# Performance work log

Hardware: AMD Instinct MI355X
Metric: run time of the kernel (lower is better)

The kernel has to match this reference:

```python
import jax, jax.numpy as jnp
import numpy as np

B, N, NODE_DIM = 256, 200, 2
H, D, L, FF = 8, 128, 3, 512
KD = D // H  # key/val dim per head = 16
EPS = 1e-5


def _uniform(key, shape, fan):
    s = 1.0 / np.sqrt(fan)
    return jax.random.uniform(key, shape, jnp.float32, -s, s)


def setup_inputs() -> dict:
    key = jax.random.key(0)
    ks = jax.random.split(key, 16)
    return {
        "x": jax.random.normal(ks[0], (B, N, NODE_DIM), jnp.float32),
        "Wemb": _uniform(ks[1], (NODE_DIM, D), NODE_DIM),
        "bemb": _uniform(ks[2], (D,), NODE_DIM),
        "Wq": _uniform(ks[3], (L, H, D, KD), KD),
        "Wk": _uniform(ks[4], (L, H, D, KD), KD),
        "Wv": _uniform(ks[5], (L, H, D, KD), KD),
        "Wo": _uniform(ks[6], (L, H, KD, D), D),
        "bn1_g": jnp.ones((L, D), jnp.float32),
        "bn1_b": jnp.zeros((L, D), jnp.float32),
        "W1": _uniform(ks[7], (L, D, FF), D),
        "b1": _uniform(ks[8], (L, FF), D),
        "W2": _uniform(ks[9], (L, FF, D), FF),
        "b2": _uniform(ks[10], (L, D), FF),
        "bn2_g": jnp.ones((L, D), jnp.float32),
        "bn2_b": jnp.zeros((L, D), jnp.float32),
    }


def _batch_norm(h, g, b):
    # BatchNorm1d in training mode: stats over all (batch*graph) positions per channel
    hf = h.reshape(-1, h.shape[-1])
    m = hf.mean(axis=0)
    v = hf.var(axis=0)  # biased variance, as torch uses for normalization
    return (h - m) * jax.lax.rsqrt(v + EPS) * g + b


def _mha(h, Wq, Wk, Wv, Wo):
    # h: [B,N,D]; Wq/Wk/Wv: [H,D,KD]; Wo: [H,KD,D]
    Q = jnp.einsum('bnd,hdk->hbnk', h, Wq)
    K = jnp.einsum('bnd,hdk->hbnk', h, Wk)
    V = jnp.einsum('bnd,hdk->hbnk', h, Wv)
    scores = jnp.einsum('hbqk,hbnk->hbqn', Q, K) * (1.0 / np.sqrt(KD))
    attn = jax.nn.softmax(scores, axis=-1)
    heads = jnp.einsum('hbqn,hbnk->hbqk', attn, V)
    return jnp.einsum('hbqk,hkd->bqd', heads, Wo)


def reference(x, Wemb, bemb, Wq, Wk, Wv, Wo, bn1_g, bn1_b, W1, b1, W2, b2, bn2_g, bn2_b):
    h = x @ Wemb + bemb  # init_embed: [B,N,D]
    for l in range(L):
        h = h + _mha(h, Wq[l], Wk[l], Wv[l], Wo[l])
        h = _batch_norm(h, bn1_g[l], bn1_b[l])
        ff = jax.nn.relu(h @ W1[l] + b1[l]) @ W2[l] + b2[l]
        h = _batch_norm(h + ff, bn2_g[l], bn2_b[l])
    return (h, h.mean(axis=1))
```

## Files before the change

### kernel.cpp

```cpp
#include <hip/hip_runtime.h>
#include <math.h>

#define B_ 256
#define N_ 200
#define D_ 128
#define H_ 8
#define KD_ 16
#define L_ 3
#define FF_ 512
#define ROWS (B_*N_)
#define BND (ROWS*D_)

typedef float f32x4 __attribute__((ext_vector_type(4)));
typedef _Float16 f16x4 __attribute__((ext_vector_type(4)));
typedef _Float16 f16x8 __attribute__((ext_vector_type(8)));

__device__ __forceinline__ ushort f2h_bits(float f) {
  _Float16 h = (_Float16)f;
  union { _Float16 h; ushort u; } v; v.h = h; return v.u;
}
__device__ __forceinline__ float h2f(ushort u) {
  union { ushort u; _Float16 h; } v; v.u = u; return (float)v.h;
}
__device__ __forceinline__ void splith(float f, ushort& hi, ushort& lo) {
  _Float16 h = (_Float16)f;
  float hf = (float)h;
  _Float16 l = (_Float16)(f - hf);
  union { _Float16 h; ushort u; } a, b; a.h = h; b.h = l;
  hi = a.u; lo = b.u;
}
__device__ __forceinline__ void bn_reduce(const float* psum, const float* psq,
    const float* gamma, const float* beta, int c, float& sc, float& sh) {
  if (gamma == nullptr) { sc = 1.f; sh = 0.f; return; }
  float s = 0.f, q = 0.f;
  for (int r = 0; r < 400; r++) { s += psum[r*128 + c]; q += psq[r*128 + c]; }
  const float invM = 1.f / 51200.f;
  float m = s * invM;
  float v = fmaf(q, invM, -m * m);
  float rr = rsqrtf(v + 1e-5f);
  sc = rr * gamma[c];
  sh = fmaf(-m, sc, beta[c]);
}

__global__ __launch_bounds__(256) void embed_kernel(const float* __restrict__ x,
    const float* __restrict__ Wemb, const float* __restrict__ bemb,
    ushort* __restrict__ hhi, ushort* __restrict__ hlo)
{
  int i4 = blockIdx.x * 256 + threadIdx.x;
  int r  = i4 >> 5, c4 = i4 & 31;
  float x0 = x[2*r], x1 = x[2*r + 1];
  const float4 w0 = ((const float4*)Wemb)[c4];
  const float4 w1 = ((const float4*)Wemb)[32 + c4];
  const float4 bb = ((const float4*)bemb)[c4];
  float o[4];
  o[0] = fmaf(x0, w0.x, fmaf(x1, w1.x, bb.x));
  o[1] = fmaf(x0, w0.y, fmaf(x1, w1.y, bb.y));
  o[2] = fmaf(x0, w0.z, fmaf(x1, w1.z, bb.z));
  o[3] = fmaf(x0, w0.w, fmaf(x1, w1.w, bb.w));
  ushort hi[4], lo[4];
#pragma unroll
  for (int k = 0; k < 4; k++) splith(o[k], hi[k], lo[k]);
  uint2 ph, pl;
  ph.x = (uint)hi[0] | ((uint)hi[1] << 16);
  ph.y = (uint)hi[2] | ((uint)hi[3] << 16);
  pl.x = (uint)lo[0] | ((uint)lo[1] << 16);
  pl.y = (uint)lo[2] | ((uint)lo[3] << 16);
  ((uint2*)hhi)[i4] = ph;
  ((uint2*)hlo)[i4] = pl;
}

__global__ __launch_bounds__(256) void t_wo(const float* __restrict__ Wo,
    ushort* __restrict__ dh)
{
  int i = blockIdx.x * 256 + threadIdx.x;
  int l = i / 16384, r = i % 16384;
  int n = r >> 7, k = r & 127;
  int hh = k >> 4, kd = k & 15;
  float w = Wo[l*16384 + hh*2048 + kd*128 + n];
  dh[i] = f2h_bits(w);
}
__global__ __launch_bounds__(256) void t_w2(const float* __restrict__ W2,
    ushort* __restrict__ dh)
{
  int i = blockIdx.x * 256 + threadIdx.x;
  int l = i / 65536, r = i % 65536;
  int d = r >> 9, f = r & 511;
  float w = W2[l*65536 + f*128 + d];
  dh[i] = f2h_bits(w);
}

__global__ __launch_bounds__(128) void fold_qkv(const float* __restrict__ Wq,
    const float* __restrict__ Wk, const float* __restrict__ Wv,
    const float* __restrict__ psum, const float* __restrict__ psq,
    const float* __restrict__ gamma, const float* __restrict__ beta,
    ushort* __restrict__ wh, float* __restrict__ bout,
    float* __restrict__ scout, float* __restrict__ shout)
{
  __shared__ float wsum[2];
  int n = blockIdx.x;
  int k = threadIdx.x;
  float sc, sh;
  bn_reduce(psum, psq, gamma, beta, k, sc, sh);
  if (n == 0) { scout[k] = sc; shout[k] = sh; }
  int which = n >> 7, hh = (n >> 4) & 7, kd = n & 15;
  const float* src = (which == 0) ? Wq : (which == 1) ? Wk : Wv;
  float w = src[hh*2048 + k*16 + kd];
  if (which == 0) w *= 0.25f * 1.44269504088896340736f;
  wh[n*128 + k] = f2h_bits(w * sc);
  float p = sh * w;
#pragma unroll
  for (int d = 1; d < 64; d <<= 1) p += __shfl_xor(p, d);
  if ((k & 63) == 0) wsum[k >> 6] = p;
  __syncthreads();
  if (k == 0) bout[n] = wsum[0] + wsum[1];
}

__global__ __launch_bounds__(128) void fold_w1(const float* __restrict__ W1,
    const float* __restrict__ b1,
    const float* __restrict__ psum, const float* __restrict__ psq,
    const float* __restrict__ gamma, const float* __restrict__ beta,
    ushort* __restrict__ wh, float* __restrict__ bout,
    float* __restrict__ scout, float* __restrict__ shout)
{
  __shared__ float wsum[2];
  int f = blockIdx.x;
  int k = threadIdx.x;
  float sc, sh;
  bn_reduce(psum, psq, gamma, beta, k, sc, sh);
  if (f == 0) { scout[k] = sc; shout[k] = sh; }
  float w = W1[k*512 + f];
  wh[f*128 + k] = f2h_bits(w * sc);
  float p = sh * w;
#pragma unroll
  for (int d = 1; d < 64; d <<= 1) p += __shfl_xor(p, d);
  if ((k & 63) == 0) wsum[k >> 6] = p;
  __syncthreads();
  if (k == 0) bout[f] = b1[f] + wsum[0] + wsum[1];
}

template<int K, bool ALO, bool BIAS, bool RELU, bool RESIDBN,
         bool OUTQKV, bool OUT16, bool OUTHL, bool STATS>
__global__ __launch_bounds__(256, 2) void gemm_mfma(
    const ushort* __restrict__ Ahi, const ushort* __restrict__ Alo,
    const ushort* __restrict__ Wh,
    const float* __restrict__ bias,
    const ushort* rhi, const ushort* rlo,
    const float* __restrict__ rsc, const float* __restrict__ rsh,
    ushort* o0, ushort* o1, ushort* o2,
    float* __restrict__ psum, float* __restrict__ psq, int Ntot)
{
  __shared__ ushort AhiS[128*64];
  __shared__ ushort AloS[ALO ? 128*64 : 8];
  __shared__ ushort BhS [128*64];
  const int t    = threadIdx.x;
  const int nx   = gridDim.x;
  const int nwg  = nx * gridDim.y;
  const int lin  = blockIdx.y * nx + blockIdx.x;
  const int q8   = nwg >> 3, r8 = nwg & 7;
  const int xcd  = lin & 7, i8 = lin >> 3;
  const int wg   = (xcd < r8 ? xcd*(q8+1) : r8*(q8+1) + (xcd-r8)*q8) + i8;
  const int bm   = (wg / nx) * 128;
  const int bn   = (wg % nx) * 128;
  const int lane = t & 63;
  const int w    = t >> 6, wm = w >> 1, wn = w & 1;
  const int quad = lane >> 4, l15 = lane & 15;
  const int bky  = wg / nx;

  f32x4 acc[4][4];
#pragma unroll
  for (int i = 0; i < 4; i++)
#pragma unroll
    for (int j = 0; j < 4; j++) acc[i][j] = (f32x4){0.f, 0.f, 0.f, 0.f};

  const ushort* AhiB = Ahi + (size_t)bm * K;
  const ushort* AloB = ALO ? (Alo + (size_t)bm * K) : nullptr;
  const ushort* BhB  = Wh  + (size_t)bn * K;

  for (int k0 = 0; k0 < K; k0 += 64) {
#pragma unroll
    for (int i = 0; i < 4; i++) {
      int idx = i * 256 + t;
      int row = idx >> 3, c = idx & 7;
      int k8  = c ^ (row & 7);
      size_t off = (size_t)row * K + k0 + k8 * 8;
      ((uint4*)AhiS)[idx] = *(const uint4*)(AhiB + off);
      if (ALO) ((uint4*)AloS)[idx] = *(const uint4*)(AloB + off);
      ((uint4*)BhS)[idx]  = *(const uint4*)(BhB + off);
    }
    __syncthreads();
#pragma unroll
    for (int ks = 0; ks < 2; ks++) {
      f16x8 ah[4], al[4], bh[4];
#pragma unroll
      for (int i = 0; i < 4; i++) {
        int row = wm * 64 + i * 16 + l15;
        int k8  = ks * 4 + quad;
        int ci  = k8 ^ (row & 7);
        ah[i] = ((const f16x8*)AhiS)[row * 8 + ci];
        if (ALO) al[i] = ((const f16x8*)AloS)[row * 8 + ci];
        int nrow = wn * 64 + i * 16 + l15;
        int cj   = k8 ^ (nrow & 7);
        bh[i] = ((const f16x8*)BhS)[nrow * 8 + cj];
      }
#pragma unroll
      for (int i = 0; i < 4; i++)
#pragma unroll
        for (int j = 0; j < 4; j++) {
          if (ALO) acc[i][j] = __builtin_amdgcn_mfma_f32_16x16x32_f16(al[i], bh[j], acc[i][j], 0, 0, 0);
          acc[i][j] = __builtin_amdgcn_mfma_f32_16x16x32_f16(ah[i], bh[j], acc[i][j], 0, 0, 0);
        }
    }
    __syncthreads();
  }

  float bv[4], scv[4], shv[4];
#pragma unroll
  for (int j = 0; j < 4; j++) {
    int col = bn + wn*64 + j*16 + l15;
    if (BIAS)    bv[j]  = bias[col];
    if (RESIDBN) { scv[j] = rsc[col]; shv[j] = rsh[col]; }
  }
  float sj[4] = {0.f,0.f,0.f,0.f}, qj[4] = {0.f,0.f,0.f,0.f};
#pragma unroll
  for (int i = 0; i < 4; i++) {
#pragma unroll
    for (int r = 0; r < 4; r++) {
      int row = bm + wm*64 + i*16 + quad*4 + r;
#pragma unroll
      for (int j = 0; j < 4; j++) {
        int col = bn + wn*64 + j*16 + l15;
        float v = acc[i][j][r];
        if (BIAS)    v += bv[j];
        if (RELU)    v = fmaxf(v, 0.f);
        if (RESIDBN) {
          size_t ri = (size_t)row * Ntot + col;
          float rr = h2f(rhi[ri]) + h2f(rlo[ri]);
          v += fmaf(rr, scv[j], shv[j]);
        }
        if (OUTQKV) {
          if (bn == 0) {
            o0[((size_t)(col >> 4) * ROWS + row) * 16 + (col & 15)] = f2h_bits(v);
          } else if (bn == 128) {
            int c = col - 128;
            o1[((size_t)(c >> 4) * ROWS + row) * 16 + (c & 15)] = f2h_bits(v);
          } else {
            int c = col - 256;
            o2[((size_t)(c >> 4) * ROWS + row) * 16 + (c & 15)] = f2h_bits(v);
          }
        }
        if (OUT16) o0[(size_t)row * Ntot + col] = f2h_bits(v);
        if (OUTHL) {
          ushort hi, lo; splith(v, hi, lo);
          o0[(size_t)row * Ntot + col] = hi;
          o1[(size_t)row * Ntot + col] = lo;
        }
        if (STATS) { sj[j] += v; qj[j] = fmaf(v, v, qj[j]); }
      }
    }
  }
  if (STATS) {
#pragma unroll
    for (int j = 0; j < 4; j++) {
      sj[j] += __shfl_xor(sj[j], 16); sj[j] += __shfl_xor(sj[j], 32);
      qj[j] += __shfl_xor(qj[j], 16); qj[j] += __shfl_xor(qj[j], 32);
    }
    float* ssum = (float*)AhiS;
    float* ssq  = ssum + 128;
    if (t < 128) { ssum[t] = 0.f; ssq[t] = 0.f; }
    __syncthreads();
    if (quad == 0) {
#pragma unroll
      for (int j = 0; j < 4; j++) {
        int col = wn*64 + j*16 + l15;
        atomicAdd(&ssum[col], sj[j]);
        atomicAdd(&ssq[col],  qj[j]);
      }
    }
    __syncthreads();
    if (t < 128) {
      psum[bky * 128 + t] = ssum[t];
      psq [bky * 128 + t] = ssq[t];
    }
  }
}

__global__ __launch_bounds__(256) void attn_kernel(const ushort* __restrict__ qs,
    const ushort* __restrict__ ks, const ushort* __restrict__ vh,
    ushort* __restrict__ hd)
{
  __shared__ __align__(16) _Float16 Ksh[208*24];
  __shared__ __align__(16) _Float16 VTh[16*216];
  const int b  = blockIdx.x >> 3;
  const int hh = blockIdx.x & 7;
  const int t  = threadIdx.x;
  const size_t rb = (size_t)b * N_;
  const size_t hb = ((size_t)hh * ROWS + rb) * 16;

  for (int i = t; i < 208*2; i += 256) {
    int n = i >> 1, half = i & 1;
    uint4 kv = {0u, 0u, 0u, 0u};
    if (n < N_) kv = *(const uint4*)(ks + hb + n*16 + half*8);
    *(uint4*)&Ksh[n*24 + half*8] = kv;
  }
  for (int i = t; i < 208*2; i += 256) {
    int n = i >> 1, half = i & 1;
    uint4 v0 = {0u, 0u, 0u, 0u};
    if (n < N_) v0 = *(const uint4*)(vh + hb + n*16 + half*8);
    const ushort* e0 = (const ushort*)&v0;
#pragma unroll
    for (int q = 0; q < 8; q++)
      ((ushort*)VTh)[(half*8 + q)*216 + n] = e0[q];
  }
  __syncthreads();

  const int lane = t & 63;
  const int w    = t >> 6;
  const int l15  = lane & 15;
  const int g    = lane >> 4;

  for (int qt = w; qt < 13; qt += 4) {
    int qr  = qt*16 + l15;
    int qrc = qr < N_ ? qr : N_-1;
    f16x4 bq = *(const f16x4*)(qs + hb + (size_t)qrc*16 + g*4);

    f32x4 ct[13];
#pragma unroll
    for (int kt = 0; kt < 13; kt++) {
      f16x4 ak = *(const f16x4*)&Ksh[(kt*16 + l15)*24 + g*4];
      ct[kt] = __builtin_amdgcn_mfma_f32_16x16x16f16(ak, bq, (f32x4){0.f,0.f,0.f,0.f}, 0, 0, 0);
    }
#pragma unroll
    for (int r = 0; r < 4; r++)
      if (g*4 + r >= 8) ct[12][r] = -1e30f;

    float m0 = -1e30f, m1 = -1e30f;
#pragma unroll
    for (int kt = 0; kt < 13; kt++) {
      m0 = fmaxf(m0, fmaxf(ct[kt][0], ct[kt][1]));
      m1 = fmaxf(m1, fmaxf(ct[kt][2], ct[kt][3]));
    }
    float m = fmaxf(m0, m1);
    m = fmaxf(m, __shfl_xor(m, 16));
    m = fmaxf(m, __shfl_xor(m, 32));

    float la0 = 0.f, la1 = 0.f, la2 = 0.f, la3 = 0.f;
#pragma unroll
    for (int kt = 0; kt < 13; kt++) {
      float p0 = __builtin_amdgcn_exp2f(ct[kt][0] - m);
      float p1 = __builtin_amdgcn_exp2f(ct[kt][1] - m);
      float p2 = __builtin_amdgcn_exp2f(ct[kt][2] - m);
      float p3 = __builtin_amdgcn_exp2f(ct[kt][3] - m);
      la0 += p0; la1 += p1; la2 += p2; la3 += p3;
      ct[kt][0] = p0; ct[kt][1] = p1; ct[kt][2] = p2; ct[kt][3] = p3;
    }
    float l = (la0 + la1) + (la2 + la3);
    l += __shfl_xor(l, 16);
    l += __shfl_xor(l, 32);

    f32x4 och = {0.f,0.f,0.f,0.f};
#pragma unroll
    for (int kt = 0; kt < 13; kt++) {
      f16x4 pt = { (_Float16)ct[kt][0], (_Float16)ct[kt][1],
                   (_Float16)ct[kt][2], (_Float16)ct[kt][3] };
      f16x4 avh = *(const f16x4*)&VTh[l15*216 + kt*16 + g*4];
      och = __builtin_amdgcn_mfma_f32_16x16x16f16(avh, pt, och, 0, 0, 0);
    }

    if (qr < N_) {
      float inv = __builtin_amdgcn_rcpf(l);
      ushort o16[4];
#pragma unroll
      for (int r = 0; r < 4; r++) o16[r] = f2h_bits(och[r] * inv);
      uint2 p;
      p.x = (uint)o16[0] | ((uint)o16[1] << 16);
      p.y = (uint)o16[2] | ((uint)o16[3] << 16);
      *(uint2*)(hd + (rb + qr)*128 + hh*16 + g*4) = p;
    }
  }
}

__global__ __launch_bounds__(128) void bn_mean_final(const ushort* __restrict__ hhi,
    const ushort* __restrict__ hlo,
    const float* __restrict__ psum, const float* __restrict__ psq,
    const float* __restrict__ gamma, const float* __restrict__ beta,
    float* __restrict__ outh, float* __restrict__ mout)
{
  int b = blockIdx.x, d = threadIdx.x;
  float sc, sh;
  bn_reduce(psum, psq, gamma, beta, d, sc, sh);
  float s = 0.f;
  for (int n = 0; n < N_; n++) {
    size_t idx = ((size_t)b * N_ + n) * 128 + d;
    float v = fmaf(h2f(hhi[idx]) + h2f(hlo[idx]), sc, sh);
    outh[idx] = v;
    s += v;
  }
  mout[b * 128 + d] = s * (1.f / N_);
}

extern "C" void kernel_launch(void* const* d_in, const int* in_sizes, int n_in,
                              void* d_out, int out_size, void* d_ws, size_t ws_size,
                              hipStream_t stream)
{
  const float* x    = (const float*)d_in[0];
  const float* Wemb = (const float*)d_in[1];
  const float* bemb = (const float*)d_in[2];
  const float* Wq   = (const float*)d_in[3];
  const float* Wk   = (const float*)d_in[4];
  const float* Wv   = (const float*)d_in[5];
  const float* Wo   = (const float*)d_in[6];
  const float* bn1g = (const float*)d_in[7];
  const float* bn1b = (const float*)d_in[8];
  const float* W1   = (const float*)d_in[9];
  const float* b1   = (const float*)d_in[10];
  const float* W2   = (const float*)d_in[11];
  const float* b2   = (const float*)d_in[12];
  const float* bn2g = (const float*)d_in[13];
  const float* bn2b = (const float*)d_in[14];
  float* out = (float*)d_out;

  char* wsb = (char*)d_ws;
  ushort* h_hi  = (ushort*)wsb;
  ushort* h_lo  = (ushort*)(wsb + 13107200);
  char*   phase = wsb + 26214400;
  ushort* qsb   = (ushort*)phase;
  ushort* ksb   = (ushort*)(phase + 13107200);
  ushort* vhh   = (ushort*)(phase + 26214400);
  ushort* hd    = (ushort*)(phase + 52428800);
  ushort* hid   = (ushort*)phase;
  char*   wp    = wsb + 91750400;
  ushort* woT   = (ushort*)wp;
  ushort* w2T   = (ushort*)(wp + 98304);
  ushort* fqkvw = (ushort*)(wp + 491520);
  ushort* fw1w  = (ushort*)(wp + 589824);
  float*  fqkv_b = (float*)(wp + 720896);
  float*  fw1_b  = (float*)(wp + 722432);
  float*  psum   = (float*)(wp + 724480);
  float*  psq    = (float*)(wp + 929280);
  float*  sc_a   = (float*)(wp + 1134080);
  float*  sh_a   = (float*)(wp + 1134592);
  float*  sc_b   = (float*)(wp + 1135104);
  float*  sh_b   = (float*)(wp + 1135616);

  embed_kernel<<<6400, 256, 0, stream>>>(x, Wemb, bemb, h_hi, h_lo);
  t_wo<<<192, 256, 0, stream>>>(Wo, woT);
  t_w2<<<768, 256, 0, stream>>>(W2, w2T);

  for (int l = 0; l < L_; l++) {
    fold_qkv<<<384, 128, 0, stream>>>(Wq + l*16384, Wk + l*16384, Wv + l*16384,
                                      psum, psq,
                                      l == 0 ? nullptr : bn2g + (l-1)*128,
                                      l == 0 ? nullptr : bn2b + (l-1)*128,
                                      fqkvw, fqkv_b, sc_b, sh_b);
    gemm_mfma<128, true, true, false, false, true, false, false, false>
        <<<dim3(3, 400), 256, 0, stream>>>(
        h_hi, h_lo, fqkvw, fqkv_b, nullptr, nullptr, nullptr, nullptr,
        qsb, ksb, vhh, nullptr, nullptr, 384);
    attn_kernel<<<B_ * H_, 256, 0, stream>>>(qsb, ksb, vhh, hd);
    gemm_mfma<128, false, false, false, true, false, false, true, true>
        <<<dim3(1, 400), 256, 0, stream>>>(
        hd, nullptr, woT + l*16384, nullptr, h_hi, h_lo, sc_b, sh_b,
        h_hi, h_lo, nullptr, psum, psq, 128);
    fold_w1<<<512, 128, 0, stream>>>(W1 + l*65536, b1 + l*512,
                                     psum, psq, bn1g + l*128, bn1b + l*128,
                                     fw1w, fw1_b, sc_a, sh_a);
    gemm_mfma<128, true, true, true, false, false, true, false, false>
        <<<dim3(4, 400), 256, 0, stream>>>(
        h_hi, h_lo, fw1w, fw1_b, nullptr, nullptr, nullptr, nullptr,
        hid, nullptr, nullptr, nullptr, nullptr, 512);
    gemm_mfma<512, false, true, false, true, false, false, true, true>
        <<<dim3(1, 400), 256, 0, stream>>>(
        hid, nullptr, w2T + l*65536, b2 + l*128, h_hi, h_lo, sc_a, sh_a,
        h_hi, h_lo, nullptr, psum, psq, 128);
  }

  bn_mean_final<<<B_, 128, 0, stream>>>(h_hi, h_lo, psum, psq,
                                        bn2g + 2*128, bn2b + 2*128, out, out + BND);
}
```

Baseline: 624.1 us.

## Drop low-half A operand in GEMMs, merge weight transposes, split final BN

The GEMMs no longer load and multiply the low fp16 residual of the activation (hi/lo split). This halves A-side LDS traffic and the MFMA count for the QKV and W1 GEMMs, at the cost of using only fp16 precision for the activation inputs. The two weight-transpose kernels are merged into one launch. The final BN/mean kernel now uses 256 threads that each cover half the rows, with a shared-memory reduction.

```diff
diff --git a/kernel.cpp b/kernel.cpp
--- a/kernel.cpp
+++ b/kernel.cpp
@@ -69,24 +69,21 @@
   ((uint2*)hlo)[i4] = pl;
 }
 
-__global__ __launch_bounds__(256) void t_wo(const float* __restrict__ Wo,
-    ushort* __restrict__ dh)
+__global__ __launch_bounds__(256) void t_weights(const float* __restrict__ Wo,
+    const float* __restrict__ W2, ushort* __restrict__ woT, ushort* __restrict__ w2T)
 {
   int i = blockIdx.x * 256 + threadIdx.x;
-  int l = i / 16384, r = i % 16384;
-  int n = r >> 7, k = r & 127;
-  int hh = k >> 4, kd = k & 15;
-  float w = Wo[l*16384 + hh*2048 + kd*128 + n];
-  dh[i] = f2h_bits(w);
-}
-__global__ __launch_bounds__(256) void t_w2(const float* __restrict__ W2,
-    ushort* __restrict__ dh)
-{
-  int i = blockIdx.x * 256 + threadIdx.x;
-  int l = i / 65536, r = i % 65536;
-  int d = r >> 9, f = r & 511;
-  float w = W2[l*65536 + f*128 + d];
-  dh[i] = f2h_bits(w);
+  if (i < 49152) {
+    int l = i / 16384, r = i % 16384;
+    int n = r >> 7, k = r & 127;
+    int hh = k >> 4, kd = k & 15;
+    woT[i] = f2h_bits(Wo[l*16384 + hh*2048 + kd*128 + n]);
+  } else {
+    int j = i - 49152;
+    int l = j / 65536, r = j % 65536;
+    int d = r >> 9, f = r & 511;
+    w2T[j] = f2h_bits(W2[l*65536 + f*128 + d]);
+  }
 }
 
 __global__ __launch_bounds__(128) void fold_qkv(const float* __restrict__ Wq,
@@ -138,10 +135,10 @@
   if (k == 0) bout[f] = b1[f] + wsum[0] + wsum[1];
 }
 
-template<int K, bool ALO, bool BIAS, bool RELU, bool RESIDBN,
+template<int K, bool BIAS, bool RELU, bool RESIDBN,
          bool OUTQKV, bool OUT16, bool OUTHL, bool STATS>
 __global__ __launch_bounds__(256, 2) void gemm_mfma(
-    const ushort* __restrict__ Ahi, const ushort* __restrict__ Alo,
+    const ushort* __restrict__ Ah,
     const ushort* __restrict__ Wh,
     const float* __restrict__ bias,
     const ushort* rhi, const ushort* rlo,
@@ -149,9 +146,8 @@
     ushort* o0, ushort* o1, ushort* o2,
     float* __restrict__ psum, float* __restrict__ psq, int Ntot)
 {
-  __shared__ ushort AhiS[128*64];
-  __shared__ ushort AloS[ALO ? 128*64 : 8];
-  __shared__ ushort BhS [128*64];
+  __shared__ ushort AhS[128*64];
+  __shared__ ushort BhS[128*64];
   const int t    = threadIdx.x;
   const int nx   = gridDim.x;
   const int nwg  = nx * gridDim.y;
@@ -172,9 +168,8 @@
 #pragma unroll
     for (int j = 0; j < 4; j++) acc[i][j] = (f32x4){0.f, 0.f, 0.f, 0.f};
 
-  const ushort* AhiB = Ahi + (size_t)bm * K;
-  const ushort* AloB = ALO ? (Alo + (size_t)bm * K) : nullptr;
-  const ushort* BhB  = Wh  + (size_t)bn * K;
+  const ushort* AhB = Ah + (size_t)bm * K;
+  const ushort* BhB = Wh + (size_t)bn * K;
 
   for (int k0 = 0; k0 < K; k0 += 64) {
 #pragma unroll
@@ -183,21 +178,19 @@
       int row = idx >> 3, c = idx & 7;
       int k8  = c ^ (row & 7);
       size_t off = (size_t)row * K + k0 + k8 * 8;
-      ((uint4*)AhiS)[idx] = *(const uint4*)(AhiB + off);
-      if (ALO) ((uint4*)AloS)[idx] = *(const uint4*)(AloB + off);
-      ((uint4*)BhS)[idx]  = *(const uint4*)(BhB + off);
+      ((uint4*)AhS)[idx] = *(const uint4*)(AhB + off);
+      ((uint4*)BhS)[idx] = *(const uint4*)(BhB + off);
     }
     __syncthreads();
 #pragma unroll
     for (int ks = 0; ks < 2; ks++) {
-      f16x8 ah[4], al[4], bh[4];
+      f16x8 ah[4], bh[4];
 #pragma unroll
       for (int i = 0; i < 4; i++) {
         int row = wm * 64 + i * 16 + l15;
         int k8  = ks * 4 + quad;
         int ci  = k8 ^ (row & 7);
-        ah[i] = ((const f16x8*)AhiS)[row * 8 + ci];
-        if (ALO) al[i] = ((const f16x8*)AloS)[row * 8 + ci];
+        ah[i] = ((const f16x8*)AhS)[row * 8 + ci];
         int nrow = wn * 64 + i * 16 + l15;
         int cj   = k8 ^ (nrow & 7);
         bh[i] = ((const f16x8*)BhS)[nrow * 8 + cj];
@@ -205,10 +198,8 @@
 #pragma unroll
       for (int i = 0; i < 4; i++)
 #pragma unroll
-        for (int j = 0; j < 4; j++) {
-          if (ALO) acc[i][j] = __builtin_amdgcn_mfma_f32_16x16x32_f16(al[i], bh[j], acc[i][j], 0, 0, 0);
+        for (int j = 0; j < 4; j++)
           acc[i][j] = __builtin_amdgcn_mfma_f32_16x16x32_f16(ah[i], bh[j], acc[i][j], 0, 0, 0);
-        }
     }
     __syncthreads();
   }
@@ -264,7 +255,7 @@
       sj[j] += __shfl_xor(sj[j], 16); sj[j] += __shfl_xor(sj[j], 32);
       qj[j] += __shfl_xor(qj[j], 16); qj[j] += __shfl_xor(qj[j], 32);
     }
-    float* ssum = (float*)AhiS;
+    float* ssum = (float*)AhS;
     float* ssq  = ssum + 128;
     if (t < 128) { ssum[t] = 0.f; ssq[t] = 0.f; }
     __syncthreads();
@@ -379,23 +370,28 @@
   }
 }
 
-__global__ __launch_bounds__(128) void bn_mean_final(const ushort* __restrict__ hhi,
+__global__ __launch_bounds__(256) void bn_mean_final(const ushort* __restrict__ hhi,
     const ushort* __restrict__ hlo,
     const float* __restrict__ psum, const float* __restrict__ psq,
     const float* __restrict__ gamma, const float* __restrict__ beta,
     float* __restrict__ outh, float* __restrict__ mout)
 {
-  int b = blockIdx.x, d = threadIdx.x;
+  __shared__ float part[2][128];
+  int b = blockIdx.x;
+  int t = threadIdx.x;
+  int d = t & 127, half = t >> 7;
   float sc, sh;
   bn_reduce(psum, psq, gamma, beta, d, sc, sh);
   float s = 0.f;
-  for (int n = 0; n < N_; n++) {
+  for (int n = half*100; n < half*100 + 100; n++) {
     size_t idx = ((size_t)b * N_ + n) * 128 + d;
     float v = fmaf(h2f(hhi[idx]) + h2f(hlo[idx]), sc, sh);
     outh[idx] = v;
     s += v;
   }
-  mout[b * 128 + d] = s * (1.f / N_);
+  part[half][d] = s;
+  __syncthreads();
+  if (half == 0) mout[b * 128 + d] = (part[0][d] + part[1][d]) * (1.f / N_);
 }
 
 extern "C" void kernel_launch(void* const* d_in, const int* in_sizes, int n_in,
@@ -443,8 +439,7 @@
   float*  sh_b   = (float*)(wp + 1135616);
 
   embed_kernel<<<6400, 256, 0, stream>>>(x, Wemb, bemb, h_hi, h_lo);
-  t_wo<<<192, 256, 0, stream>>>(Wo, woT);
-  t_w2<<<768, 256, 0, stream>>>(W2, w2T);
+  t_weights<<<960, 256, 0, stream>>>(Wo, W2, woT, w2T);
 
   for (int l = 0; l < L_; l++) {
     fold_qkv<<<384, 128, 0, stream>>>(Wq + l*16384, Wk + l*16384, Wv + l*16384,
@@ -452,28 +447,28 @@
                                       l == 0 ? nullptr : bn2g + (l-1)*128,
                                       l == 0 ? nullptr : bn2b + (l-1)*128,
                                       fqkvw, fqkv_b, sc_b, sh_b);
-    gemm_mfma<128, true, true, false, false, true, false, false, false>
+    gemm_mfma<128, true, false, false, true, false, false, false>
         <<<dim3(3, 400), 256, 0, stream>>>(
-        h_hi, h_lo, fqkvw, fqkv_b, nullptr, nullptr, nullptr, nullptr,
+        h_hi, fqkvw, fqkv_b, nullptr, nullptr, nullptr, nullptr,
         qsb, ksb, vhh, nullptr, nullptr, 384);
     attn_kernel<<<B_ * H_, 256, 0, stream>>>(qsb, ksb, vhh, hd);
-    gemm_mfma<128, false, false, false, true, false, false, true, true>
+    gemm_mfma<128, false, false, true, false, false, true, true>
         <<<dim3(1, 400), 256, 0, stream>>>(
-        hd, nullptr, woT + l*16384, nullptr, h_hi, h_lo, sc_b, sh_b,
+        hd, woT + l*16384, nullptr, h_hi, h_lo, sc_b, sh_b,
         h_hi, h_lo, nullptr, psum, psq, 128);
     fold_w1<<<512, 128, 0, stream>>>(W1 + l*65536, b1 + l*512,
                                      psum, psq, bn1g + l*128, bn1b + l*128,
                                      fw1w, fw1_b, sc_a, sh_a);
-    gemm_mfma<128, true, true, true, false, false, true, false, false>
+    gemm_mfma<128, true, true, false, false, true, false, false>
         <<<dim3(4, 400), 256, 0, stream>>>(
-        h_hi, h_lo, fw1w, fw1_b, nullptr, nullptr, nullptr, nullptr,
+        h_hi, fw1w, fw1_b, nullptr, nullptr, nullptr, nullptr,
         hid, nullptr, nullptr, nullptr, nullptr, 512);
-    gemm_mfma<512, false, true, false, true, false, false, true, true>
+    gemm_mfma<512, true, false, true, false, false, true, true>
         <<<dim3(1, 400), 256, 0, stream>>>(
-        hid, nullptr, w2T + l*65536, b2 + l*128, h_hi, h_lo, sc_a, sh_a,
+        hid, w2T + l*65536, b2 + l*128, h_hi, h_lo, sc_a, sh_a,
         h_hi, h_lo, nullptr, psum, psq, 128);
   }
 
-  bn_mean_final<<<B_, 128, 0, stream>>>(h_hi, h_lo, psum, psq,
+  bn_mean_final<<<B_, 256, 0, stream>>>(h_hi, h_lo, psum, psq,
                                         bn2g + 2*128, bn2b + 2*128, out, out + BND);
 }
```

Result: faster. 596.9 us (-4.4%).
